# Performance work log

Hardware: AMD Instinct MI355X
Metric: run time of the kernel (lower is better)

## Reference

```python
import math
import jax, jax.numpy as jnp
import numpy as np

B, H, W, DIM, HEADS, K = 4, 56, 56, 512, 16, 7


def setup_inputs() -> dict:
    key = jax.random.key(0)
    ks = jax.random.split(key, 8)
    s = 1.0 / math.sqrt(DIM)
    return {
        "hidden_states": jax.random.normal(ks[0], (B, H, W, DIM), jnp.float32),
        "Wq": jax.random.normal(ks[1], (DIM, DIM), jnp.float32) * s,
        "bq": jnp.zeros((DIM,), jnp.float32),
        "Wk": jax.random.normal(ks[2], (DIM, DIM), jnp.float32) * s,
        "bk": jnp.zeros((DIM,), jnp.float32),
        "Wv": jax.random.normal(ks[3], (DIM, DIM), jnp.float32) * s,
        "bv": jnp.zeros((DIM,), jnp.float32),
        "rpb": jax.random.normal(ks[4], (HEADS, 2 * K - 1, 2 * K - 1), jnp.float32) * 0.02,
    }


def reference(hidden_states, Wq, bq, Wk, bk, Wv, bv, rpb):
    b, h_sz, w_sz, dim = hidden_states.shape
    heads = rpb.shape[0]
    k = (rpb.shape[1] + 1) // 2  # rpb is [heads, 2k-1, 2k-1]
    d = dim // heads

    def split_heads(x):
        # [B,H,W,dim] -> [B,heads,H,W,d]  (matches transpose_for_scores permute(0,3,1,2,4))
        return x.reshape(b, h_sz, w_sz, heads, d).transpose(0, 3, 1, 2, 4)

    q = split_heads(hidden_states @ Wq.T + bq) / jnp.sqrt(jnp.asarray(d, hidden_states.dtype))
    key = split_heads(hidden_states @ Wk.T + bk)
    val = split_heads(hidden_states @ Wv.T + bv)

    half = k // 2
    ii = jnp.arange(h_sz)
    ni = jnp.clip(ii - half, 0, h_sz - k)  # neighborhood row start per query row (NATTEN edge clamping)
    jj = jnp.arange(w_sz)
    nj = jnp.clip(jj - half, 0, w_sz - k)

    # natten2dqkrpb: windowed QK with relative position bias (loop over k*k kernel offsets,
    # which mirrors the fused kernel's inner loop and avoids a [B,h,H,W,k,k,d] gather blowup)
    scores = []
    for ki in range(k):
        ridx = ni + ki                      # [H] key row index per query row
        bi = ridx - ii + (k - 1)            # [H] relative bias row index
        key_r = key[:, :, ridx]             # [B,h,H,W,d]
        rpb_r = rpb[:, bi]                  # [h,H,2k-1]
        for kj in range(k):
            cidx = nj + kj                  # [W]
            bj = cidx - jj + (k - 1)        # [W]
            key_rc = key_r[:, :, :, cidx]   # [B,h,H,W,d]
            s = jnp.einsum('bhijd,bhijd->bhij', q, key_rc)
            scores.append(s + rpb_r[:, :, bj][None])  # add bias [1,h,H,W]
    scores = jnp.stack(scores, axis=-1)     # [B,h,H,W,k*k]

    probs = jax.nn.softmax(scores, axis=-1)  # dropout p=0.0 -> identity

    # natten2dav: windowed AV
    ctx = jnp.zeros_like(q)                 # [B,h,H,W,d]
    idx = 0
    for ki in range(k):
        v_r = val[:, :, ni + ki]
        for kj in range(k):
            ctx = ctx + probs[..., idx, None] * v_r[:, :, :, nj + kj]
            idx += 1

    # permute(0,2,3,1,4) then merge heads
    return ctx.transpose(0, 2, 3, 1, 4).reshape(b, h_sz, w_sz, dim)
```

## Files before the change

kernel.cpp:

```cpp
#include <hip/hip_runtime.h>
#include <stdint.h>

typedef unsigned short u16;
typedef __bf16 bf16x8 __attribute__((ext_vector_type(8)));
typedef float f32x4 __attribute__((ext_vector_type(4)));

#define M_PIX 12544
#define DIMC  512
#define NQKV  1536

static __device__ __forceinline__ u16 f2bf(float f) {
  union { float f; uint32_t u; } x; x.f = f;
  uint32_t r = x.u + 0x7FFFu + ((x.u >> 16) & 1u);
  return (u16)(r >> 16);
}

__global__ void cast_all(const float* __restrict__ x, const float* __restrict__ Wq,
                         const float* __restrict__ Wk, const float* __restrict__ Wv,
                         u16* __restrict__ Xb, u16* __restrict__ Wc) {
  int idx = (blockIdx.x * 256 + threadIdx.x) * 4;
  const int NX = M_PIX * DIMC;
  const float* src;
  u16* dst;
  if (idx < NX) {
    src = x + idx; dst = Xb + idx;
  } else {
    int wi = idx - NX;
    if (wi >= NQKV * DIMC) return;
    int r = wi >> 9;
    int c = wi & 511;
    src = (r < 512)  ? (Wq + (size_t)r * 512 + c)
        : (r < 1024) ? (Wk + (size_t)(r - 512) * 512 + c)
                     : (Wv + (size_t)(r - 1024) * 512 + c);
    dst = Wc + wi;
  }
  float4 f = *(const float4*)src;
  uint32_t p0 = (uint32_t)f2bf(f.x) | ((uint32_t)f2bf(f.y) << 16);
  uint32_t p1 = (uint32_t)f2bf(f.z) | ((uint32_t)f2bf(f.w) << 16);
  *(uint2*)dst = make_uint2(p0, p1);
}

__global__ __launch_bounds__(256, 4) void gemm_qkv(
    const u16* __restrict__ A, const u16* __restrict__ Bm,
    const float* __restrict__ bq, const float* __restrict__ bk,
    const float* __restrict__ bv, u16* __restrict__ qkv) {
  __shared__ u16 sA[2][128 * 32];
  __shared__ u16 sB[2][128 * 32];
  const int t = threadIdx.x;
  const int lane = t & 63;
  const int w = t >> 6;
  const int tile_m = blockIdx.x * 128;
  const int tile_n = blockIdx.y * 128;
  const int wm = (w & 1) * 64;
  const int wn = (w >> 1) * 64;
  const int quad = lane >> 4;
  const int l16 = lane & 15;

  f32x4 acc[4][4];
#pragma unroll
  for (int a = 0; a < 4; ++a)
#pragma unroll
    for (int bb = 0; bb < 4; ++bb) acc[a][bb] = (f32x4){0.f, 0.f, 0.f, 0.f};

  const int c0 = t, c1 = t + 256;
  const int r0 = c0 >> 2, ko0 = (c0 & 3) * 8;
  const int r1 = c1 >> 2, ko1 = (c1 & 3) * 8;
  const u16* gA0 = A + (size_t)(tile_m + r0) * DIMC + ko0;
  const u16* gA1 = A + (size_t)(tile_m + r1) * DIMC + ko1;
  const u16* gB0 = Bm + (size_t)(tile_n + r0) * DIMC + ko0;
  const u16* gB1 = Bm + (size_t)(tile_n + r1) * DIMC + ko1;
  const int ldsoff = (t & ~63) * 8;

  for (int k0 = 0; k0 < DIMC; k0 += 64) {
#pragma unroll
    for (int h = 0; h < 2; ++h) {
      __builtin_amdgcn_global_load_lds(
          (const __attribute__((address_space(1))) void*)(gA0 + k0 + h * 32),
          (__attribute__((address_space(3))) void*)(sA[h] + 0 * 2048 + ldsoff), 16, 0, 0);
      __builtin_amdgcn_global_load_lds(
          (const __attribute__((address_space(1))) void*)(gA1 + k0 + h * 32),
          (__attribute__((address_space(3))) void*)(sA[h] + 1 * 2048 + ldsoff), 16, 0, 0);
      __builtin_amdgcn_global_load_lds(
          (const __attribute__((address_space(1))) void*)(gB0 + k0 + h * 32),
          (__attribute__((address_space(3))) void*)(sB[h] + 0 * 2048 + ldsoff), 16, 0, 0);
      __builtin_amdgcn_global_load_lds(
          (const __attribute__((address_space(1))) void*)(gB1 + k0 + h * 32),
          (__attribute__((address_space(3))) void*)(sB[h] + 1 * 2048 + ldsoff), 16, 0, 0);
    }
    __syncthreads();

#pragma unroll
    for (int h = 0; h < 2; ++h) {
      bf16x8 af[4], bfr[4];
#pragma unroll
      for (int mt = 0; mt < 4; ++mt)
        af[mt] = *(const bf16x8*)(sA[h] + (wm + mt * 16 + l16) * 32 + quad * 8);
#pragma unroll
      for (int nt = 0; nt < 4; ++nt)
        bfr[nt] = *(const bf16x8*)(sB[h] + (wn + nt * 16 + l16) * 32 + quad * 8);
#pragma unroll
      for (int mt = 0; mt < 4; ++mt)
#pragma unroll
        for (int nt = 0; nt < 4; ++nt)
          acc[mt][nt] = __builtin_amdgcn_mfma_f32_16x16x32_bf16(bfr[nt], af[mt], acc[mt][nt], 0, 0, 0);
    }
    __syncthreads();
  }

  const float qscale = 0.17677669529663687f;
#pragma unroll
  for (int mt = 0; mt < 4; ++mt) {
    const int m = tile_m + wm + mt * 16 + l16;
#pragma unroll
    for (int nt = 0; nt < 4; ++nt) {
      const int n0 = tile_n + wn + nt * 16 + quad * 4;
      const int mat = n0 >> 9;
      const int cc = n0 & 511;
      const float* bias = (mat == 0) ? bq : (mat == 1) ? bk : bv;
      const float4 bv4 = *(const float4*)(bias + cc);
      const float scl = (mat == 0) ? qscale : 1.0f;
      u16 h0 = f2bf((acc[mt][nt][0] + bv4.x) * scl);
      u16 h1 = f2bf((acc[mt][nt][1] + bv4.y) * scl);
      u16 h2 = f2bf((acc[mt][nt][2] + bv4.z) * scl);
      u16 h3 = f2bf((acc[mt][nt][3] + bv4.w) * scl);
      uint2 pk = make_uint2((uint32_t)h0 | ((uint32_t)h1 << 16),
                            (uint32_t)h2 | ((uint32_t)h3 << 16));
      *(uint2*)(qkv + (size_t)mat * M_PIX * DIMC + (size_t)m * DIMC + cc) = pk;
    }
  }
}

__global__ __launch_bounds__(256, 4) void natten_k(const u16* __restrict__ qkv,
                                                   const float* __restrict__ rpb,
                                                   float* __restrict__ out) {
  __shared__ u16 uShared[11360];
  __shared__ u16 sVt[32 * 232];
  __shared__ float sRpb[176];
  __shared__ uint32_t sTbl[320];
  u16* sK = uShared;
  u16* sQ = uShared + 8800;
  u16* sP = uShared;

  const int tid = threadIdx.x;
  const int lane = tid & 63;
  const int w = tid >> 6;
  const int l16 = lane & 15;
  const int quad = lane >> 4;

  const int bid = blockIdx.x;
  const int xcd = bid & 7;
  const int idx = bid >> 3;
  const int head = idx / 28;
  const int gl = idx - head * 28;
  const int g = xcd * 28 + gl;
  const int jg = g & 3;
  const int gi = g >> 2;
  const int b = gi / 14;
  const int ig = gi - b * 14;
  const int i0 = ig * 4, j0 = jg * 14;
  int c0 = j0 - 3; c0 = c0 < 0 ? 0 : (c0 > 36 ? 36 : c0);
  int nib = i0 - 3; nib = nib < 0 ? 0 : (nib > 49 ? 49 : nib);

  const int iw = i0 + w;
  int niw = iw - 3; niw = niw < 0 ? 0 : (niw > 49 ? 49 : niw);
  const int rowoff = niw - nib;
  const int par = rowoff & 1;
  const int woff2 = rowoff * 20 - par * 4;
  const int wconst = niw - iw + 6;

  const int qv = l16 < 14 ? l16 : 13;
  const int jq = j0 + qv;
  int njq = jq - 3; njq = njq < 0 ? 0 : (njq > 49 ? 49 : njq);
  const uint32_t offq = (uint32_t)(njq - c0);
  const int Cq = wconst * 13 + (c0 - jq + 6);

  const u16* Kpl = qkv + (size_t)M_PIX * DIMC;

  for (int it = 0; it < 4; ++it) {
    int task = it * 256 + tid;
    if (task < 880) {
      int cand = task >> 2, dg = task & 3;
      int r = (cand * 205) >> 12;
      int c = cand - r * 20;
      int rimg = nib + r;
      uint4 kk = make_uint4(0, 0, 0, 0);
      if (rimg < 56) {
        size_t px = (size_t)((b * 56 + rimg) * 56 + c0 + c);
        kk = *(const uint4*)(Kpl + px * DIMC + head * 32 + dg * 8);
      }
      *(uint4*)((char*)sK + cand * 80 + dg * 16) = kk;
    }
  }
  {
    const int cand = tid;
    if (cand < 220) {
      int r = (cand * 205) >> 12;
      int c = cand - r * 20;
      int rimg = nib + r;
      const bool ok = (rimg < 56);
      size_t px = (size_t)((b * 56 + rimg) * 56 + c0 + c);
      const u16* vsrc = Kpl + (size_t)M_PIX * DIMC + px * DIMC + head * 32;
      u16* vt = sVt + cand;
#pragma unroll
      for (int dg = 0; dg < 4; ++dg) {
        uint4 vv = ok ? *(const uint4*)(vsrc + dg * 8) : make_uint4(0, 0, 0, 0);
        int d0 = dg * 8;
        vt[(d0 + 0) * 232] = (u16)(vv.x & 0xFFFF); vt[(d0 + 1) * 232] = (u16)(vv.x >> 16);
        vt[(d0 + 2) * 232] = (u16)(vv.y & 0xFFFF); vt[(d0 + 3) * 232] = (u16)(vv.y >> 16);
        vt[(d0 + 4) * 232] = (u16)(vv.z & 0xFFFF); vt[(d0 + 5) * 232] = (u16)(vv.z >> 16);
        vt[(d0 + 6) * 232] = (u16)(vv.w & 0xFFFF); vt[(d0 + 7) * 232] = (u16)(vv.w >> 16);
      }
    }
  }
  {
    u16* sQw = sQ + w * 640;
    if (lane < 56) {
      int q = lane >> 2, dg = lane & 3;
      size_t px = (size_t)((b * 56 + iw) * 56 + j0 + q);
      uint4 qq = *(const uint4*)(qkv + px * DIMC + head * 32 + dg * 8);
      *(uint4*)((char*)sQw + q * 80 + dg * 16) = qq;
    } else {
      int tq = lane - 56;
      int q = 14 + (tq >> 2), dg = tq & 3;
      *(uint4*)((char*)sQw + q * 80 + dg * 16) = make_uint4(0, 0, 0, 0);
    }
  }
  if (tid < 169) sRpb[tid] = rpb[head * 169 + tid];
  for (int s2 = tid; s2 < 320; s2 += 256) {
    int pp = s2 >= 160 ? 1 : 0;
    int s = s2 - pp * 160;
    int t0 = s - pp * 4;
    uint32_t e = 255u;
    if (t0 >= 0 && t0 < 140) {
      int r = (t0 * 205) >> 12;
      int c = t0 - r * 20;
      e = (uint32_t)c | ((uint32_t)(r * 13 + c) << 8);
    }
    sTbl[s2] = e;
  }
  __syncthreads();

  u16* sQw = sQ + w * 640;
  u16* sPw = sP + w * 2688;
  const bf16x8 qf = *(const bf16x8*)((char*)sQw + l16 * 80 + quad * 16);
  f32x4 S[10];
#pragma unroll
  for (int ch = 0; ch < 10; ++ch) {
    bf16x8 kf = *(const bf16x8*)((char*)sK + (woff2 + ch * 16 + l16) * 80 + quad * 16);
    S[ch] = __builtin_amdgcn_mfma_f32_16x16x32_bf16(kf, qf, (f32x4){0.f, 0.f, 0.f, 0.f}, 0, 0, 0);
  }

  __syncthreads();

  const float LOG2E = 1.4426950408889634f;
  float l = 0.f;
  const uint32_t* tb = sTbl + par * 160;
#pragma unroll
  for (int ch = 0; ch < 10; ++ch) {
    uint4 te = *(const uint4*)(tb + ch * 16 + quad * 4);
    float pv[4];
    uint32_t es[4] = {te.x, te.y, te.z, te.w};
#pragma unroll
    for (int rg = 0; rg < 4; ++rg) {
      uint32_t e = es[rg];
      uint32_t ce = e & 255u;
      bool valid = (ce - offq) < 7u;
      int ridx = valid ? (int)((e >> 8) & 255u) + Cq : 0;
      float rb = sRpb[ridx];
      float p = exp2f((S[ch][rg] + rb) * LOG2E);
      p = valid ? p : 0.f;
      pv[rg] = p;
      l += p;
    }
    uint2 pk = make_uint2((uint32_t)f2bf(pv[0]) | ((uint32_t)f2bf(pv[1]) << 16),
                          (uint32_t)f2bf(pv[2]) | ((uint32_t)f2bf(pv[3]) << 16));
    *(uint2*)((char*)sPw + l16 * 336 + ch * 32 + quad * 8) = pk;
  }
  l += __shfl_xor(l, 16);
  l += __shfl_xor(l, 32);

  __syncthreads();

  f32x4 O0 = (f32x4){0.f, 0.f, 0.f, 0.f};
  f32x4 O1 = (f32x4){0.f, 0.f, 0.f, 0.f};
#pragma unroll
  for (int c32 = 0; c32 < 5; ++c32) {
    bf16x8 pf = *(const bf16x8*)((char*)sPw + l16 * 336 + c32 * 64 + quad * 16);
    bf16x8 v0 = *(const bf16x8*)((char*)sVt + (0 + l16) * 464 + woff2 * 2 + c32 * 64 + quad * 16);
    bf16x8 v1 = *(const bf16x8*)((char*)sVt + (16 + l16) * 464 + woff2 * 2 + c32 * 64 + quad * 16);
    O0 = __builtin_amdgcn_mfma_f32_16x16x32_bf16(v0, pf, O0, 0, 0, 0);
    O1 = __builtin_amdgcn_mfma_f32_16x16x32_bf16(v1, pf, O1, 0, 0, 0);
  }

  if (l16 < 14) {
    const float inv = 1.0f / l;
    float* op = out + ((size_t)((b * 56 + iw) * 56 + j0 + l16)) * DIMC + head * 32;
    *(float4*)(op + quad * 4) =
        make_float4(O0[0] * inv, O0[1] * inv, O0[2] * inv, O0[3] * inv);
    *(float4*)(op + 16 + quad * 4) =
        make_float4(O1[0] * inv, O1[1] * inv, O1[2] * inv, O1[3] * inv);
  }
}

extern "C" void kernel_launch(void* const* d_in, const int* in_sizes, int n_in,
                              void* d_out, int out_size, void* d_ws, size_t ws_size,
                              hipStream_t stream) {
  const float* x   = (const float*)d_in[0];
  const float* Wq  = (const float*)d_in[1];
  const float* bq  = (const float*)d_in[2];
  const float* Wk  = (const float*)d_in[3];
  const float* bk  = (const float*)d_in[4];
  const float* Wv  = (const float*)d_in[5];
  const float* bv  = (const float*)d_in[6];
  const float* rpb = (const float*)d_in[7];
  float* out = (float*)d_out;

  u16* Xb  = (u16*)d_ws;
  u16* Wc  = Xb + (size_t)M_PIX * DIMC;
  u16* qkv = Wc + (size_t)NQKV * DIMC;

  const int ncast = (M_PIX * DIMC + NQKV * DIMC) / 4;
  cast_all<<<(ncast + 255) / 256, 256, 0, stream>>>(x, Wq, Wk, Wv, Xb, Wc);
  dim3 g(M_PIX / 128, NQKV / 128);
  gemm_qkv<<<g, 256, 0, stream>>>(Xb, Wc, bq, bk, bv, qkv);
  natten_k<<<16 * 224, 256, 0, stream>>>(qkv, rpb, out);
}
```

Measured before the change: 161.4 us.

## Restructure QKV GEMM with 256x128 tiles, double-buffered prefetch, swizzled LDS, XCD remap

The QKV projection GEMM now uses 512-thread blocks computing 256x128 tiles over full 64-wide K chunks. The next chunk is prefetched into a second LDS buffer in two halves, interleaved with the MFMA phases and guarded by s_setprio and barriers. LDS columns are XOR-swizzled to avoid bank conflicts, and block IDs are remapped across the 8 XCDs so neighbouring tiles share L2. This trades a larger LDS footprint and lower occupancy for better overlap of loads with compute and more reuse.

New measurement: 174.4 us. +8.1%, slower.

```diff
diff --git a/kernel.cpp b/kernel.cpp
--- a/kernel.cpp
+++ b/kernel.cpp
@@ -40,80 +40,93 @@
   *(uint2*)dst = make_uint2(p0, p1);
 }
 
-__global__ __launch_bounds__(256, 4) void gemm_qkv(
+static __device__ __forceinline__ void gemm_phase(
+    const u16* pA, const u16* pB, int wmOff, int wnOff, int l16, int quad,
+    int p, f32x4 acc[4][4]) {
+  const int cb = (((p) * 4 + quad) ^ (l16 & 7)) << 4;
+  bf16x8 aF[4], bF[4];
+#pragma unroll
+  for (int i = 0; i < 4; ++i) {
+    aF[i] = *(const bf16x8*)((const char*)pA + (wmOff + i * 16 + l16) * 128 + cb);
+    bF[i] = *(const bf16x8*)((const char*)pB + (wnOff + i * 16 + l16) * 128 + cb);
+  }
+  __builtin_amdgcn_s_barrier();
+  __builtin_amdgcn_s_setprio(1);
+#pragma unroll
+  for (int mt = 0; mt < 4; ++mt)
+#pragma unroll
+    for (int nt = 0; nt < 4; ++nt)
+      acc[mt][nt] = __builtin_amdgcn_mfma_f32_16x16x32_bf16(bF[nt], aF[mt], acc[mt][nt], 0, 0, 0);
+  __builtin_amdgcn_s_setprio(0);
+  __builtin_amdgcn_s_barrier();
+}
+
+__global__ __launch_bounds__(512, 2) void gemm_qkv(
     const u16* __restrict__ A, const u16* __restrict__ Bm,
     const float* __restrict__ bq, const float* __restrict__ bk,
     const float* __restrict__ bv, u16* __restrict__ qkv) {
-  __shared__ u16 sA[2][128 * 32];
-  __shared__ u16 sB[2][128 * 32];
+  __shared__ u16 sA[2][256 * 64];
+  __shared__ u16 sB[2][128 * 64];
   const int t = threadIdx.x;
   const int lane = t & 63;
   const int w = t >> 6;
-  const int tile_m = blockIdx.x * 128;
-  const int tile_n = blockIdx.y * 128;
-  const int wm = (w & 1) * 64;
-  const int wn = (w >> 1) * 64;
+  const int l16 = lane & 15;
   const int quad = lane >> 4;
-  const int l16 = lane & 15;
+
+  const int orig = blockIdx.x;
+  const int xcd = orig & 7, loc = orig >> 3;
+  const int wg = (xcd < 4) ? xcd * 74 + loc : 296 + (xcd - 4) * 73 + loc;
+  const int mtile = wg % 49, ntile = wg / 49;
+  const int tile_m = mtile * 256, tile_n = ntile * 128;
+
+  const int wmOff = (w & 3) * 64;
+  const int wnOff = (w >> 2) * 64;
+
+  const int rloc = t >> 3, slot = t & 7;
+  const int scol = (slot ^ (rloc & 7)) * 8;
+  const u16* gA = A + (size_t)(tile_m + rloc) * DIMC + scol;
+  const u16* gB = Bm + (size_t)(tile_n + rloc) * DIMC + scol;
+  const int ldsoff = (t & ~63) * 8;
 
   f32x4 acc[4][4];
 #pragma unroll
   for (int a = 0; a < 4; ++a)
 #pragma unroll
-    for (int bb = 0; bb < 4; ++bb) acc[a][bb] = (f32x4){0.f, 0.f, 0.f, 0.f};
-
-  const int c0 = t, c1 = t + 256;
-  const int r0 = c0 >> 2, ko0 = (c0 & 3) * 8;
-  const int r1 = c1 >> 2, ko1 = (c1 & 3) * 8;
-  const u16* gA0 = A + (size_t)(tile_m + r0) * DIMC + ko0;
-  const u16* gA1 = A + (size_t)(tile_m + r1) * DIMC + ko1;
-  const u16* gB0 = Bm + (size_t)(tile_n + r0) * DIMC + ko0;
-  const u16* gB1 = Bm + (size_t)(tile_n + r1) * DIMC + ko1;
-  const int ldsoff = (t & ~63) * 8;
-
-  for (int k0 = 0; k0 < DIMC; k0 += 64) {
-#pragma unroll
-    for (int h = 0; h < 2; ++h) {
-      __builtin_amdgcn_global_load_lds(
-          (const __attribute__((address_space(1))) void*)(gA0 + k0 + h * 32),
-          (__attribute__((address_space(3))) void*)(sA[h] + 0 * 2048 + ldsoff), 16, 0, 0);
-      __builtin_amdgcn_global_load_lds(
-          (const __attribute__((address_space(1))) void*)(gA1 + k0 + h * 32),
-          (__attribute__((address_space(3))) void*)(sA[h] + 1 * 2048 + ldsoff), 16, 0, 0);
-      __builtin_amdgcn_global_load_lds(
-          (const __attribute__((address_space(1))) void*)(gB0 + k0 + h * 32),
-          (__attribute__((address_space(3))) void*)(sB[h] + 0 * 2048 + ldsoff), 16, 0, 0);
-      __builtin_amdgcn_global_load_lds(
-          (const __attribute__((address_space(1))) void*)(gB1 + k0 + h * 32),
-          (__attribute__((address_space(3))) void*)(sB[h] + 1 * 2048 + ldsoff), 16, 0, 0);
-    }
+    for (int b = 0; b < 4; ++b) acc[a][b] = (f32x4){0.f, 0.f, 0.f, 0.f};
+
+#define STG_A(buf, ch, kc)                                                         \
+  __builtin_amdgcn_global_load_lds(                                                \
+      (const __attribute__((address_space(1))) void*)(gA + (size_t)(ch) * 64 * DIMC + (kc)), \
+      (__attribute__((address_space(3))) void*)(sA[buf] + (ch) * 4096 + ldsoff), 16, 0, 0)
+#define STG_B(buf, ch, kc)                                                         \
+  __builtin_amdgcn_global_load_lds(                                                \
+      (const __attribute__((address_space(1))) void*)(gB + (size_t)(ch) * 64 * DIMC + (kc)), \
+      (__attribute__((address_space(3))) void*)(sB[buf] + (ch) * 4096 + ldsoff), 16, 0, 0)
+
+  STG_A(0, 0, 0); STG_A(0, 1, 0); STG_A(0, 2, 0); STG_A(0, 3, 0);
+  STG_B(0, 0, 0); STG_B(0, 1, 0);
+
+  for (int kt = 0; kt < 8; ++kt) {
+    const int cur = kt & 1;
     __syncthreads();
-
-#pragma unroll
-    for (int h = 0; h < 2; ++h) {
-      bf16x8 af[4], bfr[4];
-#pragma unroll
-      for (int mt = 0; mt < 4; ++mt)
-        af[mt] = *(const bf16x8*)(sA[h] + (wm + mt * 16 + l16) * 32 + quad * 8);
-#pragma unroll
-      for (int nt = 0; nt < 4; ++nt)
-        bfr[nt] = *(const bf16x8*)(sB[h] + (wn + nt * 16 + l16) * 32 + quad * 8);
-#pragma unroll
-      for (int mt = 0; mt < 4; ++mt)
-#pragma unroll
-        for (int nt = 0; nt < 4; ++nt)
-          acc[mt][nt] = __builtin_amdgcn_mfma_f32_16x16x32_bf16(bfr[nt], af[mt], acc[mt][nt], 0, 0, 0);
-    }
-    __syncthreads();
+    const u16* pA = sA[cur];
+    const u16* pB = sB[cur];
+    const int nxt = cur ^ 1;
+    const int kc = (kt + 1) * 64;
+    const bool pf = (kt < 7);
+    if (pf) { STG_A(nxt, 0, kc); STG_A(nxt, 1, kc); STG_B(nxt, 0, kc); }
+    gemm_phase(pA, pB, wmOff, wnOff, l16, quad, 0, acc);
+    if (pf) { STG_A(nxt, 2, kc); STG_A(nxt, 3, kc); STG_B(nxt, 1, kc); }
+    gemm_phase(pA, pB, wmOff, wnOff, l16, quad, 1, acc);
   }
 
   const float qscale = 0.17677669529663687f;
 #pragma unroll
   for (int mt = 0; mt < 4; ++mt) {
-    const int m = tile_m + wm + mt * 16 + l16;
+    const int m = tile_m + wmOff + mt * 16 + l16;
 #pragma unroll
     for (int nt = 0; nt < 4; ++nt) {
-      const int n0 = tile_n + wn + nt * 16 + quad * 4;
+      const int n0 = tile_n + wnOff + nt * 16 + quad * 4;
       const int mat = n0 >> 9;
       const int cc = n0 & 511;
       const float* bias = (mat == 0) ? bq : (mat == 1) ? bk : bv;
@@ -321,7 +334,6 @@
 
   const int ncast = (M_PIX * DIMC + NQKV * DIMC) / 4;
   cast_all<<<(ncast + 255) / 256, 256, 0, stream>>>(x, Wq, Wk, Wv, Xb, Wc);
-  dim3 g(M_PIX / 128, NQKV / 128);
-  gemm_qkv<<<g, 256, 0, stream>>>(Xb, Wc, bq, bk, bv, qkv);
+  gemm_qkv<<<588, 512, 0, stream>>>(Xb, Wc, bq, bk, bv, qkv);
   natten_k<<<16 * 224, 256, 0, stream>>>(qkv, rpb, out);
 }
```
